# Performance work log

Measured on AMD Instinct MI355X. Metric: run time of the kernel, lower is better.

The kernel has to match this reference:

```python
import jax, jax.numpy as jnp
import numpy as np

NHEAD = 16


def setup_inputs() -> dict:
    key = jax.random.key(0)
    ks = jax.random.split(key, 8)
    S, B, D = 2048, 2, 1024
    std = 1.0 / np.sqrt(D)
    src = jax.random.normal(ks[0], (S, B, D), dtype=jnp.float32)
    edge_bias_2d = jax.random.normal(ks[1], (S, S), dtype=jnp.float32)
    wq = jax.random.normal(ks[2], (D, D), dtype=jnp.float32) * std
    wk = jax.random.normal(ks[3], (D, D), dtype=jnp.float32) * std
    wv = jax.random.normal(ks[4], (D, D), dtype=jnp.float32) * std
    wo = jax.random.normal(ks[5], (D, D), dtype=jnp.float32) * std
    bq = jnp.zeros((D,), jnp.float32)
    bk = jnp.zeros((D,), jnp.float32)
    bv = jnp.zeros((D,), jnp.float32)
    bo = jnp.zeros((D,), jnp.float32)
    return {"src": src, "edge_bias_2d": edge_bias_2d, "wq": wq, "bq": bq,
            "wk": wk, "bk": bk, "wv": wv, "bv": bv, "wo": wo, "bo": bo}


def reference(src, edge_bias_2d, wq, bq, wk, bk, wv, bv, wo, bo):
    S, B, D = src.shape
    h = NHEAD
    hd = D // h
    scale = hd ** (-0.5)

    def heads(t):  # [S,B,D] -> [B,h,S,hd]
        return t.reshape(S, B, h, hd).transpose(1, 2, 0, 3)

    q = heads(src @ wq + bq)
    k = heads(src @ wk + bk)
    v = heads(src @ wv + bv)

    # [B,h,S,S]
    logits = jnp.einsum('bhsd,bhtd->bhst', q, k) * scale
    logits = logits + edge_bias_2d[None, None, :, :]
    attn = jax.nn.softmax(logits, axis=-1)
    # signed aggregation: sign(edge_bias) with 0 -> +1
    sign_gate = jnp.where(edge_bias_2d < 0, -1.0, 1.0).astype(attn.dtype)
    attn = attn * sign_gate[None, None, :, :]

    out = jnp.einsum('bhst,bhtd->bhsd', attn, v)  # [B,h,S,hd]
    out = out.transpose(2, 0, 1, 3).reshape(S, B, D)
    out = out @ wo + bo
    return out
```

## Files before the change

kernel.cpp:

```cpp
#include <hip/hip_runtime.h>
#include <stdint.h>

typedef unsigned short u16;
typedef unsigned int u32;

typedef __bf16 bf8 __attribute__((ext_vector_type(8)));
typedef bf8 bf8a __attribute__((may_alias));
typedef float f32x4 __attribute__((ext_vector_type(4)));
typedef uint2 uint2a __attribute__((may_alias));
typedef ushort4 ushort4a __attribute__((may_alias));
typedef float4 float4a __attribute__((may_alias));

#define MFMA_BF16(a, b, c) __builtin_amdgcn_mfma_f32_16x16x32_bf16((a), (b), (c), 0, 0, 0)

__device__ __forceinline__ u16 f2b(float x) {
  u32 u = __float_as_uint(x);
  return (u16)((u + 0x7fffu + ((u >> 16) & 1u)) >> 16);
}
__device__ __forceinline__ void async16(const u16* g, void* l) {
  __builtin_amdgcn_global_load_lds((const __attribute__((address_space(1))) u32*)g,
                                   (__attribute__((address_space(3))) u32*)l, 16, 0, 0);
}

__global__ __launch_bounds__(256) void prep_inputs(
    const float* __restrict__ src, u16* __restrict__ dst,
    const float* __restrict__ w0, const float* __restrict__ w1,
    const float* __restrict__ w2, const float* __restrict__ w3,
    u16* __restrict__ t0, u16* __restrict__ t1, u16* __restrict__ t2, u16* __restrict__ t3) {
  const int bid = blockIdx.x, tid = threadIdx.x;
  if (bid < 4096) {
    const int i = bid * 256 + tid;
    float4 v = *(const float4a*)(src + i * 4);
    ushort4 o;
    o.x = f2b(v.x); o.y = f2b(v.y); o.z = f2b(v.z); o.w = f2b(v.w);
    *(ushort4a*)(dst + i * 4) = o;
    return;
  }
  const int b2 = bid - 4096;
  const int z = b2 >> 8, xy = b2 & 255;
  const int bx = xy & 15, by = xy >> 4;
  const float* W = z == 0 ? w0 : z == 1 ? w1 : z == 2 ? w2 : w3;
  u16* T = z == 0 ? t0 : z == 1 ? t1 : z == 2 ? t2 : t3;
  __shared__ __align__(8) u16 tile[64][68];
  const int ty = tid >> 4, tx = tid & 15;
  const int kb = by * 64, nb = bx * 64;
#pragma unroll
  for (int i = 0; i < 4; ++i) {
    int lk = ty + i * 16;
    float4 v = *(const float4a*)(W + (kb + lk) * 1024 + nb + tx * 4);
    ushort4 h;
    h.x = f2b(v.x); h.y = f2b(v.y); h.z = f2b(v.z); h.w = f2b(v.w);
    *(ushort4a*)&tile[lk][tx * 4] = h;
  }
  __syncthreads();
#pragma unroll
  for (int i = 0; i < 4; ++i) {
    int ln = ty + i * 16;
    ushort4 v;
    v.x = tile[tx * 4 + 0][ln];
    v.y = tile[tx * 4 + 1][ln];
    v.z = tile[tx * 4 + 2][ln];
    v.w = tile[tx * 4 + 3][ln];
    *(ushort4a*)(T + (nb + ln) * 1024 + kb + tx * 4) = v;
  }
}

__global__ __launch_bounds__(256) void prep_eb(const float* __restrict__ EB,
                                               u16* __restrict__ E2) {
  const int gid = blockIdx.x * 256 + threadIdx.x;
  const int s = gid >> 9;
  const int t = (gid & 511) * 4;
  const float4 v = *(const float4a*)(EB + s * 2048 + t);
  const float c2 = 1.44269504088896340736f;
  ushort4 o;
  o.x = f2b(__builtin_amdgcn_exp2f(v.x * c2)) | (u16)((__float_as_uint(v.x) >> 16) & 0x8000u);
  o.y = f2b(__builtin_amdgcn_exp2f(v.y * c2)) | (u16)((__float_as_uint(v.y) >> 16) & 0x8000u);
  o.z = f2b(__builtin_amdgcn_exp2f(v.z * c2)) | (u16)((__float_as_uint(v.z) >> 16) & 0x8000u);
  o.w = f2b(__builtin_amdgcn_exp2f(v.w * c2)) | (u16)((__float_as_uint(v.w) >> 16) & 0x8000u);
  const int ti = ((s >> 4) * 128 + (t >> 4)) * 256 + (s & 15) * 16 + (t & 15);
  *(ushort4a*)(E2 + ti) = o;
}

__global__ __launch_bounds__(256) void gemm_bt(
    const u16* __restrict__ A,
    const u16* __restrict__ B0, const u16* __restrict__ B1, const u16* __restrict__ B2,
    const float* __restrict__ c0, const float* __restrict__ c1, const float* __restrict__ c2,
    float sc0, float sc1, float sc2,
    u16* __restrict__ O0, u16* __restrict__ O1, u16* __restrict__ O2,
    float* __restrict__ Of, int plain) {
  __shared__ __align__(16) u16 sm[8192];
  u16* As = sm;
  u16* Bs = sm + 4096;
  const int tid = threadIdx.x, lane = tid & 63, w = tid >> 6;
  const int wm = w >> 1, wn = w & 1, quad = lane >> 4, l16 = lane & 15;
  const int z = blockIdx.z;
  const u16* Bt = z == 0 ? B0 : (z == 1 ? B1 : B2);
  const float* bi = z == 0 ? c0 : (z == 1 ? c1 : c2);
  const float sc = z == 0 ? sc0 : (z == 1 ? sc1 : sc2);
  u16* O = z == 0 ? O0 : (z == 1 ? O1 : O2);
  const int row0 = blockIdx.y * 128, col0 = blockIdx.x * 128;

  f32x4 acc[4][4];
#pragma unroll
  for (int i = 0; i < 4; ++i)
#pragma unroll
    for (int j = 0; j < 4; ++j) acc[i][j] = f32x4{0.f, 0.f, 0.f, 0.f};

  const int e0 = tid, e1 = tid + 256;
  const int r0 = e0 >> 2, cc0 = (e0 & 3) * 8;
  const int r1 = e1 >> 2, cc1 = (e1 & 3) * 8;
  const u32 lb0 = (u32)(w * 64) * 16;
  const u32 lb1 = (u32)(w * 64 + 256) * 16;

  for (int k0 = 0; k0 < 1024; k0 += 32) {
    __syncthreads();
    async16(A + (row0 + r0) * 1024 + k0 + cc0, (char*)As + lb0);
    async16(A + (row0 + r1) * 1024 + k0 + cc1, (char*)As + lb1);
    async16(Bt + (col0 + r0) * 1024 + k0 + cc0, (char*)Bs + lb0);
    async16(Bt + (col0 + r1) * 1024 + k0 + cc1, (char*)Bs + lb1);
    __syncthreads();
    bf8a af[4], bfr[4];
#pragma unroll
    for (int i = 0; i < 4; ++i) {
      af[i] = *(const bf8a*)(As + (wm * 64 + i * 16 + l16) * 32 + quad * 8);
      bfr[i] = *(const bf8a*)(Bs + (wn * 64 + i * 16 + l16) * 32 + quad * 8);
    }
#pragma unroll
    for (int mt = 0; mt < 4; ++mt)
#pragma unroll
      for (int nt = 0; nt < 4; ++nt) acc[mt][nt] = MFMA_BF16(af[mt], bfr[nt], acc[mt][nt]);
  }

#pragma unroll
  for (int nt = 0; nt < 4; ++nt) {
    const int col = col0 + wn * 64 + nt * 16 + l16;
    const float bcol = bi[col];
#pragma unroll
    for (int mt = 0; mt < 4; ++mt) {
#pragma unroll
      for (int r = 0; r < 4; ++r) {
        const int rm = row0 + wm * 64 + mt * 16 + quad * 4 + r;
        const float fv = (acc[mt][nt][r] + bcol) * sc;
        if (plain) {
          Of[rm * 1024 + col] = fv;
        } else {
          const u16 hv = f2b(fv);
          const int s = rm >> 1, b_ = rm & 1, hh = col >> 6, e = col & 63;
          const int p = b_ * 16 + hh;
          if (z < 2) O[(p * 2048 + s) * 64 + e] = hv;
          else O[(p * 64 + e) * 2048 + s] = hv;
        }
      }
    }
  }
}

#define STAGE_K(Ksbuf)                                                              \
  {                                                                                 \
    _Pragma("unroll") for (int c = 0; c < 4; ++c)                                   \
      async16(kpt + c * 512, (char*)(Ksbuf) + c * 1024);                            \
    kpt += 8192;                                                                    \
  }

#define ITER(KsC, KsN, vfP, vfC, FIRST, LAST)                                       \
  {                                                                                 \
             \
                            \
    asm volatile("s_waitcnt vmcnt(4)" ::: "memory");                                \
    __builtin_amdgcn_sched_barrier(0);                                              \
    bf8a pf[4];                                                                     \
    if (!(FIRST)) {                                                                 \
      _Pragma("unroll") for (int st = 0; st < 4; ++st)                              \
        pf[st] = *(const bf8a*)(Pw + st * 1152 + l16 * 72 + quad * 16);             \
    }                                                                               \
    bf8a kf[2][2];                                                                  \
    _Pragma("unroll") for (int tt = 0; tt < 2; ++tt) {                              \
      const int rl_ = tt * 16 + l16;                 \
      _Pragma("unroll") for (int ks = 0; ks < 2; ++ks) {                            \
        const int cc_ = ((ks * 4 + quad) ^ (l16 & 7)) * 8;                          \
        kf[tt][ks] = *(const bf8a*)((KsC) + rl_ * 64 + cc_);                        \
      }                                                                             \
    }                                                                               \
    if (!(LAST)) STAGE_K(KsN)                                                       \
    uint2 ebt[4][2];                                                                \
    _Pragma("unroll") for (int st = 0; st < 4; ++st)                                \
      _Pragma("unroll") for (int tt = 0; tt < 2; ++tt)                              \
        ebt[st][tt] = *(const uint2a*)(ebpt + st * 32768 + tt * 256);               \
    ebpt += 2048;                                                                   \
    f32x4 sacc[4][2];                                                               \
    __builtin_amdgcn_s_setprio(1);                                                  \
    _Pragma("unroll") for (int tt = 0; tt < 2; ++tt)                                \
      _Pragma("unroll") for (int st = 0; st < 4; ++st) {                            \
        f32x4 t0_ = f32x4{0.f, 0.f, 0.f, 0.f};                                      \
        t0_ = MFMA_BF16(kf[tt][0], qf[st][0], t0_);                                 \
        sacc[st][tt] = MFMA_BF16(kf[tt][1], qf[st][1], t0_);                        \
      }                                                                             \
    if (!(FIRST)) {           \
      _Pragma("unroll") for (int st = 0; st < 4; ++st)                              \
        _Pragma("unroll") for (int nt = 0; nt < 4; ++nt)                            \
          oacc[st][nt] = MFMA_BF16(vfP[nt], pf[st], oacc[st][nt]);                  \
    }                                                                               \
    __builtin_amdgcn_s_setprio(0);                                                  \
    _Pragma("unroll") for (int st = 0; st < 4; ++st) {                              \
      _Pragma("unroll") for (int tt = 0; tt < 2; ++tt) {                            \
        const uint2 e_ = ebt[st][tt];                                               \
        const float g0 = __uint_as_float(e_.x << 16);                               \
        const float g1 = __uint_as_float(e_.x & 0xffff0000u);                       \
        const float g2 = __uint_as_float(e_.y << 16);                               \
        const float g3 = __uint_as_float(e_.y & 0xffff0000u);                       \
        const float p0 = __builtin_amdgcn_exp2f(sacc[st][tt][0]) * g0;              \
        const float p1 = __builtin_amdgcn_exp2f(sacc[st][tt][1]) * g1;              \
        const float p2 = __builtin_amdgcn_exp2f(sacc[st][tt][2]) * g2;              \
        const float p3 = __builtin_amdgcn_exp2f(sacc[st][tt][3]) * g3;              \
        lsum[st] += (__builtin_fabsf(p0) + __builtin_fabsf(p1)) +                   \
                    (__builtin_fabsf(p2) + __builtin_fabsf(p3));                    \
        const u16 h0 = __builtin_bit_cast(u16, (__bf16)p0);                         \
        const u16 h1 = __builtin_bit_cast(u16, (__bf16)p1);                         \
        const u16 h2 = __builtin_bit_cast(u16, (__bf16)p2);                         \
        const u16 h3 = __builtin_bit_cast(u16, (__bf16)p3);                         \
        uint2 v_;                                                                   \
        v_.x = (u32)h0 | ((u32)h1 << 16);                                           \
        v_.y = (u32)h2 | ((u32)h3 << 16);                                           \
        *(uint2a*)(Pw + st * 1152 + l16 * 72 + tt * 32 + quad * 8) = v_;            \
      }                                                                             \
    }                                                                               \
    {            \
      _Pragma("unroll") for (int nt = 0; nt < 4; ++nt)                              \
        vfC[nt] = *(const bf8a*)(vpt + nt * 32768);                                 \
      vpt += 128;                                                                   \
    }                                                                               \
  }

__global__ __launch_bounds__(256, 2) void attn_fused(
    const u16* __restrict__ Qw, const u16* __restrict__ Kw, const u16* __restrict__ Vw,
    const u16* __restrict__ EBp, u16* __restrict__ Ao) {
  __shared__ __align__(16) char smem[51456];
  const int tid = threadIdx.x, lane = tid & 63, w = tid >> 6;
  const int quad = lane >> 4, l16 = lane & 15;
  const int id = blockIdx.x;
  const int xcd = id & 7, idx = id >> 3;
  const int pair = xcd * 4 + (idx & 3);
  const int qt = idx >> 2;
  const int bb = pair >> 4, hh = pair & 15;
  const u16* Qp = Qw + pair * (2048 * 64);
  const u16* Kp = Kw + pair * (2048 * 64);
  const u16* Vp = Vw + pair * (64 * 2048);
  const int s0 = qt * 64;
  u16* const Ks0 = (u16*)(smem + w * 8192);
  u16* const Ks1 = (u16*)(smem + w * 8192 + 4096);
  char* const Pw = smem + 32768 + w * 4608;

  bf8a qf[4][2];
#pragma unroll
  for (int st = 0; st < 4; ++st)
#pragma unroll
    for (int ks = 0; ks < 2; ++ks)
      qf[st][ks] = *(const bf8a*)(Qp + (s0 + st * 16 + l16) * 64 + ks * 32 + quad * 8);

  f32x4 oacc[4][4];
#pragma unroll
  for (int i = 0; i < 4; ++i)
#pragma unroll
    for (int j = 0; j < 4; ++j) oacc[i][j] = f32x4{0.f, 0.f, 0.f, 0.f};
  float lsum[4] = {0.f, 0.f, 0.f, 0.f};

  const int r8 = lane >> 3;
  const int c16s = (lane & 7) ^ r8;
  const u16* kpt = Kp + (w * 32 + r8) * 64 + c16s * 8;
  const u16* ebpt = EBp + (qt * 4 * 128 + w * 2) * 256 + l16 * 16 + quad * 4;
  const u16* vpt = Vp + l16 * 2048 + w * 32 + quad * 8;

  bf8a vfA[4], vfB[4];

  STAGE_K(Ks0)
  asm volatile("s_waitcnt vmcnt(0)" ::: "memory");
  __builtin_amdgcn_sched_barrier(0);

  ITER(Ks0, Ks1, vfA , vfA, 1, 0)
  for (int it = 0; it < 7; ++it) {
    ITER(Ks1, Ks0, vfA, vfB, 0, 0)
    ITER(Ks0, Ks1, vfB, vfA, 0, 0)
  }
  ITER(Ks1, Ks0, vfA, vfB, 0, 1)
  {
    bf8a pf[4];
#pragma unroll
    for (int st = 0; st < 4; ++st)
      pf[st] = *(const bf8a*)(Pw + st * 1152 + l16 * 72 + quad * 16);
    __builtin_amdgcn_s_setprio(1);
#pragma unroll
    for (int st = 0; st < 4; ++st)
#pragma unroll
      for (int nt = 0; nt < 4; ++nt)
        oacc[st][nt] = MFMA_BF16(vfB[nt], pf[st], oacc[st][nt]);
    __builtin_amdgcn_s_setprio(0);
  }

  __syncthreads();
  float* const Obuf = (float*)smem;
  float* const Lbuf = (float*)(smem + 51200);
#pragma unroll
  for (int st = 0; st < 4; ++st) {
    float ls = lsum[st];
    ls += __shfl_xor(ls, 16);
    ls += __shfl_xor(ls, 32);
    if (lane < 16) Lbuf[w * 16 + l16] = ls;
#pragma unroll
    for (int nt = 0; nt < 4; ++nt)
      *(float4a*)&Obuf[w * 1056 + l16 * 66 + nt * 16 + quad * 4] = (float4){
          oacc[st][nt][0], oacc[st][nt][1], oacc[st][nt][2], oacc[st][nt][3]};
    __syncthreads();
    {
      const int s_ = tid & 15, eg = (tid >> 4) * 4;
      float a0 = 0.f, a1 = 0.f, a2 = 0.f, a3 = 0.f;
#pragma unroll
      for (int wp = 0; wp < 4; ++wp) {
        const float4 x = *(const float4a*)&Obuf[wp * 1056 + s_ * 66 + eg];
        a0 += x.x; a1 += x.y; a2 += x.z; a3 += x.w;
      }
      const float lt = Lbuf[s_] + Lbuf[16 + s_] + Lbuf[32 + s_] + Lbuf[48 + s_];
      const float inv = 1.0f / lt;
      ushort4 o;
      o.x = f2b(a0 * inv); o.y = f2b(a1 * inv); o.z = f2b(a2 * inv); o.w = f2b(a3 * inv);
      *(ushort4a*)(Ao + ((s0 + st * 16 + s_) * 2 + bb) * 1024 + hh * 64 + eg) = o;
    }
    if (st < 3) __syncthreads();
  }
}

extern "C" void kernel_launch(void* const* d_in, const int* in_sizes, int n_in,
                              void* d_out, int out_size, void* d_ws, size_t ws_size,
                              hipStream_t stream) {
  const float* src = (const float*)d_in[0];
  const float* eb = (const float*)d_in[1];
  const float* wq = (const float*)d_in[2];
  const float* bq = (const float*)d_in[3];
  const float* wk = (const float*)d_in[4];
  const float* bk = (const float*)d_in[5];
  const float* wv = (const float*)d_in[6];
  const float* bv = (const float*)d_in[7];
  const float* wo = (const float*)d_in[8];
  const float* bo = (const float*)d_in[9];
  u16* ws = (u16*)d_ws;
  const size_t MM = 1024 * 1024;
  u16* wqT = ws;
  u16* wkT = ws + MM;
  u16* wvT = ws + 2 * MM;
  u16* woT = ws + 3 * MM;
  u16* srcB = ws + 4 * MM;
  u16* eb2 = ws + 4 * MM;
  u16* qW = ws + 8 * MM;
  u16* kW = ws + 12 * MM;
  u16* vW = ws + 16 * MM;
  u16* aO = ws + 20 * MM;
  float* out = (float*)d_out;
  const float c1 = 0.125f * 1.44269504088896340736f;

  prep_inputs<<<dim3(5120), 256, 0, stream>>>(src, srcB, wq, wk, wv, wo,
                                              wqT, wkT, wvT, woT);
  gemm_bt<<<dim3(8, 32, 3), 256, 0, stream>>>(srcB, wqT, wkT, wvT, bq, bk, bv,
                                              c1, 1.0f, 1.0f,
                                              qW, kW, vW, nullptr, 0);
  prep_eb<<<dim3(4096), 256, 0, stream>>>(eb, eb2);
  attn_fused<<<dim3(1024), 256, 0, stream>>>(qW, kW, vW, eb2, aO);
  gemm_bt<<<dim3(8, 32, 1), 256, 0, stream>>>(aO, woT, woT, woT, bo, bo, bo,
                                              1.0f, 1.0f, 1.0f,
                                              nullptr, nullptr, nullptr, out, 1);
}
```

Measured before the change: 251.1 us.

## Triple-buffer GEMM LDS loads and fold edge-bias prep into input prep

```diff
diff --git a/kernel.cpp b/kernel.cpp
--- a/kernel.cpp
+++ b/kernel.cpp
@@ -26,7 +26,8 @@
     const float* __restrict__ src, u16* __restrict__ dst,
     const float* __restrict__ w0, const float* __restrict__ w1,
     const float* __restrict__ w2, const float* __restrict__ w3,
-    u16* __restrict__ t0, u16* __restrict__ t1, u16* __restrict__ t2, u16* __restrict__ t3) {
+    u16* __restrict__ t0, u16* __restrict__ t1, u16* __restrict__ t2, u16* __restrict__ t3,
+    const float* __restrict__ EB, u16* __restrict__ E2) {
   const int bid = blockIdx.x, tid = threadIdx.x;
   if (bid < 4096) {
     const int i = bid * 256 + tid;
@@ -36,6 +37,21 @@
     *(ushort4a*)(dst + i * 4) = o;
     return;
   }
+  if (bid >= 5120) {
+    const int gid = (bid - 5120) * 256 + tid;
+    const int s = gid >> 9;
+    const int t = (gid & 511) * 4;
+    const float4 v = *(const float4a*)(EB + s * 2048 + t);
+    const float c2 = 1.44269504088896340736f;
+    ushort4 o;
+    o.x = f2b(__builtin_amdgcn_exp2f(v.x * c2)) | (u16)((__float_as_uint(v.x) >> 16) & 0x8000u);
+    o.y = f2b(__builtin_amdgcn_exp2f(v.y * c2)) | (u16)((__float_as_uint(v.y) >> 16) & 0x8000u);
+    o.z = f2b(__builtin_amdgcn_exp2f(v.z * c2)) | (u16)((__float_as_uint(v.z) >> 16) & 0x8000u);
+    o.w = f2b(__builtin_amdgcn_exp2f(v.w * c2)) | (u16)((__float_as_uint(v.w) >> 16) & 0x8000u);
+    const int ti = ((s >> 4) * 128 + (t >> 4)) * 256 + (s & 15) * 16 + (t & 15);
+    *(ushort4a*)(E2 + ti) = o;
+    return;
+  }
   const int b2 = bid - 4096;
   const int z = b2 >> 8, xy = b2 & 255;
   const int bx = xy & 15, by = xy >> 4;
@@ -65,21 +81,29 @@
   }
 }
 
-__global__ __launch_bounds__(256) void prep_eb(const float* __restrict__ EB,
-                                               u16* __restrict__ E2) {
-  const int gid = blockIdx.x * 256 + threadIdx.x;
-  const int s = gid >> 9;
-  const int t = (gid & 511) * 4;
-  const float4 v = *(const float4a*)(EB + s * 2048 + t);
-  const float c2 = 1.44269504088896340736f;
-  ushort4 o;
-  o.x = f2b(__builtin_amdgcn_exp2f(v.x * c2)) | (u16)((__float_as_uint(v.x) >> 16) & 0x8000u);
-  o.y = f2b(__builtin_amdgcn_exp2f(v.y * c2)) | (u16)((__float_as_uint(v.y) >> 16) & 0x8000u);
-  o.z = f2b(__builtin_amdgcn_exp2f(v.z * c2)) | (u16)((__float_as_uint(v.z) >> 16) & 0x8000u);
-  o.w = f2b(__builtin_amdgcn_exp2f(v.w * c2)) | (u16)((__float_as_uint(v.w) >> 16) & 0x8000u);
-  const int ti = ((s >> 4) * 128 + (t >> 4)) * 256 + (s & 15) * 16 + (t & 15);
-  *(ushort4a*)(E2 + ti) = o;
-}
+#define G_STAGE(base, kk)                                                           \
+  {                                                                                 \
+    u16* As_ = sm + (base);                                                         \
+    u16* Bs_ = As_ + 4096;                                                          \
+    async16(A + (row0 + r0) * 1024 + (kk) + cc0, (char*)As_ + lb0);                 \
+    async16(A + (row0 + r1) * 1024 + (kk) + cc1, (char*)As_ + lb1);                 \
+    async16(Bt + (col0 + r0) * 1024 + (kk) + cc0, (char*)Bs_ + lb0);                \
+    async16(Bt + (col0 + r1) * 1024 + (kk) + cc1, (char*)Bs_ + lb1);                \
+  }
+
+#define G_COMPUTE(base)                                                             \
+  {                                                                                 \
+    const u16* As_ = sm + (base);                                                   \
+    const u16* Bs_ = As_ + 4096;                                                    \
+    bf8a af[4], bfr[4];                                                             \
+    _Pragma("unroll") for (int i_ = 0; i_ < 4; ++i_) {                              \
+      af[i_] = *(const bf8a*)(As_ + (wm * 64 + i_ * 16 + l16) * 32 + quad * 8);     \
+      bfr[i_] = *(const bf8a*)(Bs_ + (wn * 64 + i_ * 16 + l16) * 32 + quad * 8);    \
+    }                                                                               \
+    _Pragma("unroll") for (int mt = 0; mt < 4; ++mt)                                \
+      _Pragma("unroll") for (int nt = 0; nt < 4; ++nt)                              \
+        acc[mt][nt] = MFMA_BF16(af[mt], bfr[nt], acc[mt][nt]);                      \
+  }
 
 __global__ __launch_bounds__(256) void gemm_bt(
     const u16* __restrict__ A,
@@ -88,9 +112,7 @@
     float sc0, float sc1, float sc2,
     u16* __restrict__ O0, u16* __restrict__ O1, u16* __restrict__ O2,
     float* __restrict__ Of, int plain) {
-  __shared__ __align__(16) u16 sm[8192];
-  u16* As = sm;
-  u16* Bs = sm + 4096;
+  __shared__ __align__(16) u16 sm[24576];
   const int tid = threadIdx.x, lane = tid & 63, w = tid >> 6;
   const int wm = w >> 1, wn = w & 1, quad = lane >> 4, l16 = lane & 15;
   const int z = blockIdx.z;
@@ -112,24 +134,24 @@
   const u32 lb0 = (u32)(w * 64) * 16;
   const u32 lb1 = (u32)(w * 64 + 256) * 16;
 
-  for (int k0 = 0; k0 < 1024; k0 += 32) {
-    __syncthreads();
-    async16(A + (row0 + r0) * 1024 + k0 + cc0, (char*)As + lb0);
-    async16(A + (row0 + r1) * 1024 + k0 + cc1, (char*)As + lb1);
-    async16(Bt + (col0 + r0) * 1024 + k0 + cc0, (char*)Bs + lb0);
-    async16(Bt + (col0 + r1) * 1024 + k0 + cc1, (char*)Bs + lb1);
-    __syncthreads();
-    bf8a af[4], bfr[4];
-#pragma unroll
-    for (int i = 0; i < 4; ++i) {
-      af[i] = *(const bf8a*)(As + (wm * 64 + i * 16 + l16) * 32 + quad * 8);
-      bfr[i] = *(const bf8a*)(Bs + (wn * 64 + i * 16 + l16) * 32 + quad * 8);
-    }
-#pragma unroll
-    for (int mt = 0; mt < 4; ++mt)
-#pragma unroll
-      for (int nt = 0; nt < 4; ++nt) acc[mt][nt] = MFMA_BF16(af[mt], bfr[nt], acc[mt][nt]);
-  }
+  G_STAGE(0, 0)
+  G_STAGE(8192, 32)
+  u32 bcur = 0, bnxt2 = 16384;
+  for (int i = 0; i < 31; ++i) {
+    asm volatile("s_waitcnt vmcnt(4)" ::: "memory");
+    __builtin_amdgcn_sched_barrier(0);
+    __builtin_amdgcn_s_barrier();
+    __builtin_amdgcn_sched_barrier(0);
+    if (i < 30) G_STAGE(bnxt2, (i + 2) * 32)
+    G_COMPUTE(bcur)
+    bcur = bcur == 16384 ? 0 : bcur + 8192;
+    bnxt2 = bnxt2 == 16384 ? 0 : bnxt2 + 8192;
+  }
+  asm volatile("s_waitcnt vmcnt(0)" ::: "memory");
+  __builtin_amdgcn_sched_barrier(0);
+  __builtin_amdgcn_s_barrier();
+  __builtin_amdgcn_sched_barrier(0);
+  G_COMPUTE(bcur)
 
 #pragma unroll
   for (int nt = 0; nt < 4; ++nt) {
@@ -164,8 +186,6 @@
 
 #define ITER(KsC, KsN, vfP, vfC, FIRST, LAST)                                       \
   {                                                                                 \
-             \
-                            \
     asm volatile("s_waitcnt vmcnt(4)" ::: "memory");                                \
     __builtin_amdgcn_sched_barrier(0);                                              \
     bf8a pf[4];                                                                     \
@@ -348,20 +368,19 @@
   u16* wvT = ws + 2 * MM;
   u16* woT = ws + 3 * MM;
   u16* srcB = ws + 4 * MM;
-  u16* eb2 = ws + 4 * MM;
   u16* qW = ws + 8 * MM;
   u16* kW = ws + 12 * MM;
   u16* vW = ws + 16 * MM;
   u16* aO = ws + 20 * MM;
   float* out = (float*)d_out;
+  u16* eb2 = (u16*)d_out;
   const float c1 = 0.125f * 1.44269504088896340736f;
 
-  prep_inputs<<<dim3(5120), 256, 0, stream>>>(src, srcB, wq, wk, wv, wo,
-                                              wqT, wkT, wvT, woT);
+  prep_inputs<<<dim3(9216), 256, 0, stream>>>(src, srcB, wq, wk, wv, wo,
+                                              wqT, wkT, wvT, woT, eb, eb2);
   gemm_bt<<<dim3(8, 32, 3), 256, 0, stream>>>(srcB, wqT, wkT, wvT, bq, bk, bv,
                                               c1, 1.0f, 1.0f,
                                               qW, kW, vW, nullptr, 0);
-  prep_eb<<<dim3(4096), 256, 0, stream>>>(eb, eb2);
   attn_fused<<<dim3(1024), 256, 0, stream>>>(qW, kW, vW, eb2, aO);
   gemm_bt<<<dim3(8, 32, 1), 256, 0, stream>>>(aO, woT, woT, woT, bo, bo, bo,
                                               1.0f, 1.0f, 1.0f,
```

Result: no change. 252.0 us (+0.4%).
